# Kernel optimization log

Measured on AMD Instinct MI355X. Metric: run time of the kernel, lower is better.

## Reference

```python
import jax, jax.numpy as jnp
import numpy as np

B, W, L, J, I, O = 512, 1024, 64, 8, 32, 128


def setup_inputs() -> dict:
    key = jax.random.key(0)
    ks = jax.random.split(key, 9)
    wm = jax.random.normal(ks[0], (B, W, L), dtype=jnp.float32)
    constants = jax.random.uniform(ks[1], (J, L), minval=-1.0, maxval=1.0, dtype=jnp.float32)
    gammas = jax.random.uniform(ks[2], (J, L), minval=0.0, maxval=1.0, dtype=jnp.float32)
    body_w = jax.random.normal(ks[3], (J, I, L), dtype=jnp.float32) / np.sqrt(L).astype(np.float32)
    body_b = jax.random.normal(ks[4], (J, I), dtype=jnp.float32) * 0.01
    slot_w = jax.random.normal(ks[5], (J, L * I, L), dtype=jnp.float32) / np.sqrt(L).astype(np.float32)
    slot_b = jax.random.normal(ks[6], (J, L * I), dtype=jnp.float32) * 0.01
    head_w = jax.random.normal(ks[7], (O, I), dtype=jnp.float32) / np.sqrt(I).astype(np.float32)
    head_b = jax.random.normal(ks[8], (O,), dtype=jnp.float32) * 0.01
    return {"working_memory": wm, "constants": constants, "gammas": gammas,
            "body_w": body_w, "body_b": body_b, "slot_w": slot_w, "slot_b": slot_b,
            "head_w": head_w, "head_b": head_b}


def reference(working_memory, constants, gammas, body_w, body_b, slot_w, slot_b, head_w, head_b):
    temperature = 1.0
    g = jnp.clip(gammas, 0.0, 1.0)            # (J,L), torch.clamp equivalent
    w1 = 1.0 - g                               # per-element weight (1-gamma)
    # match_scores[j,b,w] = sum_l w1[j,l] * (c[j,l] - wm[b,w,l])^2, expanded to
    # avoid materializing a (J,B,W,L) intermediate:
    A = jnp.sum(w1 * constants * constants, axis=1)                      # (J,)
    cross = jnp.einsum('jl,bwl->jbw', w1 * constants, working_memory)    # (J,B,W)
    quad = jnp.einsum('jl,bwl->jbw', w1, working_memory * working_memory)
    scores = A[:, None, None] - 2.0 * cross + quad                       # (J,B,W)
    attn = jax.nn.softmax(-scores / temperature, axis=-1)                # (J,B,W)
    best = jnp.einsum('jbw,bwl->jbl', attn, working_memory)              # (J,B,L)
    total_mq = jnp.sum(attn * scores, axis=-1).sum(axis=0)               # (B,)
    # body: per-premise Linear(L->I), scaled by mean clamped gamma
    captured = jnp.einsum('jbl,jil->jbi', best, body_w) + body_b[:, None, :]
    g_avg = g.mean(axis=1)                                               # (J,)
    captured_vars = jnp.einsum('j,jbi->bi', g_avg, captured)             # (B,I)
    # slot selector: per-premise Linear(L -> L*I), softmax over slots,
    # scatter best_props values into slots (the original inner l-loop).
    slot_logits = jnp.einsum('jbl,jkl->jbk', best, slot_w) + slot_b[:, None, :]
    slot_probs = jax.nn.softmax(slot_logits.reshape(J, -1, L, I), axis=-1)
    captured_vars = captured_vars + jnp.einsum('jbli,jbl->bi', slot_probs, best)
    output = captured_vars @ head_w.T + head_b                           # (B,O)
    confidence = jnp.exp(-total_mq)[:, None]                             # (B,1)
    return confidence * output
```

## Files before the change

kernel.cpp:

```cpp
#include <hip/hip_runtime.h>
#include <cstdint>
#include <cstddef>

#define B_ 512
#define W_ 1024
#define L_ 64
#define J_ 8
#define I_ 32
#define O_ 128


__global__ __launch_bounds__(64) void k0_prep(const float* __restrict__ constants,
    const float* __restrict__ gammas, float* __restrict__ wcg,
    float* __restrict__ w1g, float* __restrict__ Ag)
{
  const int l = threadIdx.x;
  #pragma unroll
  for (int j = 0; j < J_; ++j) {
    float g = gammas[j*L_ + l];
    g = fminf(fmaxf(g, 0.f), 1.f);
    float c = constants[j*L_ + l];
    float w1 = 1.f - g;
    w1g[j*L_ + l] = w1;
    wcg[j*L_ + l] = w1 * c;
  }
  if (l < J_) {
    float a = 0.f;
    for (int c = 0; c < L_; ++c) {
      float g = gammas[l*L_ + c];
      g = fminf(fmaxf(g, 0.f), 1.f);
      float cc = constants[l*L_ + c];
      a += (1.f - g) * cc * cc;
    }
    Ag[l] = a;
  }
}

__global__ __launch_bounds__(256, 2) void k12_fused(const float* __restrict__ wm,
    const float* __restrict__ wcg, const float* __restrict__ w1g,
    const float* __restrict__ Ag, float* __restrict__ bpart, float* __restrict__ stats)
{
  __shared__ __align__(16) float xs[128 * 68];
  __shared__ __align__(16) float es[J_ * 128];
  __shared__ float redA[4][4], redB[4][4];
  __shared__ float bcast[J_];

  const int tid = threadIdx.x;
  const int b = blockIdx.x, h = blockIdx.y;
  const int lane = tid & 63, wv = tid >> 6;
  const int w = tid & 127;
  const int jh = tid >> 7;
  const int jbase = __builtin_amdgcn_readfirstlane(jh << 2);
  const int lq = tid & 15, wsl = tid >> 4;

  float accb[J_][4];
  #pragma unroll
  for (int j = 0; j < J_; ++j)
    #pragma unroll
    for (int q = 0; q < 4; ++q) accb[j][q] = 0.f;
  float esum[4], msum[4], m0[4];
  #pragma unroll
  for (int jj = 0; jj < 4; ++jj) { esum[jj] = 0.f; msum[jj] = 0.f; }

  const float* wmb = wm + (size_t)b * (W_*L_) + (size_t)h * (512*L_);

  for (int ch = 0; ch < 4; ++ch) {
    __syncthreads();
    const float4* src = (const float4*)(wmb + ch * (128*L_));
    #pragma unroll
    for (int k = 0; k < 8; ++k) {
      int f = k*256 + tid;
      float4 v = src[f];
      int rw = f >> 4, lw = f & 15;
      *(float4*)&xs[rw*68 + lw*4] = v;
    }
    __syncthreads();

    float a1[4], a2[4];
    #pragma unroll
    for (int jj = 0; jj < 4; ++jj) { a1[jj] = 0.f; a2[jj] = 0.f; }
    #pragma unroll
    for (int c = 0; c < 16; ++c) {
      float4 x = *(const float4*)&xs[w*68 + c*4];
      float4 xq;
      xq.x = x.x*x.x; xq.y = x.y*x.y; xq.z = x.z*x.z; xq.w = x.w*x.w;
      #pragma unroll
      for (int jj = 0; jj < 4; ++jj) {
        float4 wc4 = *(const float4*)(wcg + (jbase+jj)*L_ + c*4);
        float4 w14 = *(const float4*)(w1g + (jbase+jj)*L_ + c*4);
        a1[jj] = fmaf(wc4.x, x.x, a1[jj]);
        a1[jj] = fmaf(wc4.y, x.y, a1[jj]);
        a1[jj] = fmaf(wc4.z, x.z, a1[jj]);
        a1[jj] = fmaf(wc4.w, x.w, a1[jj]);
        a2[jj] = fmaf(w14.x, xq.x, a2[jj]);
        a2[jj] = fmaf(w14.y, xq.y, a2[jj]);
        a2[jj] = fmaf(w14.z, xq.z, a2[jj]);
        a2[jj] = fmaf(w14.w, xq.w, a2[jj]);
      }
    }
    float s[4];
    #pragma unroll
    for (int jj = 0; jj < 4; ++jj)
      s[jj] = Ag[jbase+jj] - 2.f*a1[jj] + a2[jj];

    if (ch == 0) {
      #pragma unroll
      for (int jj = 0; jj < 4; ++jj) {
        float mn = s[jj];
        #pragma unroll
        for (int off = 1; off < 64; off <<= 1)
          mn = fminf(mn, __shfl_xor(mn, off));
        if (lane == 0) redA[wv][jj] = mn;
      }
      __syncthreads();
      if (tid < J_) {
        int jj = tid & 3;
        bcast[tid] = (tid < 4) ? fminf(redA[0][jj], redA[1][jj])
                               : fminf(redA[2][jj], redA[3][jj]);
      }
      __syncthreads();
      #pragma unroll
      for (int jj = 0; jj < 4; ++jj) m0[jj] = bcast[jbase+jj];
    }

    #pragma unroll
    for (int jj = 0; jj < 4; ++jj) {
      float e = __expf(m0[jj] - s[jj]);
      esum[jj] += e;
      msum[jj] = fmaf(e, s[jj], msum[jj]);
      es[(jbase+jj)*128 + w] = e;
    }
    __syncthreads();

    #pragma unroll
    for (int tg = 0; tg < 2; ++tg) {
      float4 x[4];
      #pragma unroll
      for (int t = 0; t < 4; ++t)
        x[t] = *(const float4*)&xs[(wsl*8 + tg*4 + t)*68 + lq*4];
      #pragma unroll
      for (int j = 0; j < J_; ++j) {
        float4 e4 = *(const float4*)&es[j*128 + wsl*8 + tg*4];
        accb[j][0] = fmaf(e4.x, x[0].x, accb[j][0]);
        accb[j][1] = fmaf(e4.x, x[0].y, accb[j][1]);
        accb[j][2] = fmaf(e4.x, x[0].z, accb[j][2]);
        accb[j][3] = fmaf(e4.x, x[0].w, accb[j][3]);
        accb[j][0] = fmaf(e4.y, x[1].x, accb[j][0]);
        accb[j][1] = fmaf(e4.y, x[1].y, accb[j][1]);
        accb[j][2] = fmaf(e4.y, x[1].z, accb[j][2]);
        accb[j][3] = fmaf(e4.y, x[1].w, accb[j][3]);
        accb[j][0] = fmaf(e4.z, x[2].x, accb[j][0]);
        accb[j][1] = fmaf(e4.z, x[2].y, accb[j][1]);
        accb[j][2] = fmaf(e4.z, x[2].z, accb[j][2]);
        accb[j][3] = fmaf(e4.z, x[2].w, accb[j][3]);
        accb[j][0] = fmaf(e4.w, x[3].x, accb[j][0]);
        accb[j][1] = fmaf(e4.w, x[3].y, accb[j][1]);
        accb[j][2] = fmaf(e4.w, x[3].z, accb[j][2]);
        accb[j][3] = fmaf(e4.w, x[3].w, accb[j][3]);
      }
    }
  }

  #pragma unroll
  for (int jj = 0; jj < 4; ++jj) {
    float e = esum[jj], m = msum[jj];
    #pragma unroll
    for (int off = 1; off < 64; off <<= 1) {
      e += __shfl_xor(e, off);
      m += __shfl_xor(m, off);
    }
    if (lane == 0) { redA[wv][jj] = e; redB[wv][jj] = m; }
  }
  __syncthreads();
  if (tid < J_) {
    int jj = tid & 3;
    float E = (tid < 4) ? redA[0][jj] + redA[1][jj] : redA[2][jj] + redA[3][jj];
    float M = (tid < 4) ? redB[0][jj] + redB[1][jj] : redB[2][jj] + redB[3][jj];
    float* st = stats + (((size_t)h*B_ + b)*J_ + tid)*4;
    st[0] = bcast[tid]; st[1] = E; st[2] = M;
  }

  #pragma unroll
  for (int j = 0; j < J_; ++j)
    *(float4*)&xs[((wsl*J_ + j)*16 + lq)*4] = *(float4*)accb[j];
  __syncthreads();
  if (tid < J_*16) {
    int j = tid >> 4, q = tid & 15;
    float4 sum = make_float4(0.f, 0.f, 0.f, 0.f);
    #pragma unroll
    for (int s2 = 0; s2 < 16; ++s2) {
      float4 p = *(const float4*)&xs[((s2*J_ + j)*16 + q)*4];
      sum.x += p.x; sum.y += p.y; sum.z += p.z; sum.w += p.w;
    }
    *(float4*)&bpart[(((size_t)h*J_ + j)*B_ + b)*L_ + q*4] = sum;
  }
}

__global__ __launch_bounds__(128) void k2b_combine(const float* __restrict__ bpart,
    const float* __restrict__ stats, float* __restrict__ best, float* __restrict__ conf)
{
  __shared__ float mred[J_];
  const int b = blockIdx.x, tid = threadIdx.x;
  const int j = tid >> 4, q = tid & 15;
  const float* st0 = stats + ((size_t)b*J_ + j)*4;
  const float* st1 = stats + (((size_t)B_ + b)*J_ + j)*4;
  float m0a = st0[0], E0 = st0[1], M0 = st0[2];
  float m0b = st1[0], E1 = st1[1], M1 = st1[2];
  float M = fminf(m0a, m0b);
  float s0 = __expf(M - m0a), s1 = __expf(M - m0b);
  float E = s0*E0 + s1*E1;
  float inv = 1.f / E;
  float4 p0 = *(const float4*)&bpart[((size_t)j*B_ + b)*L_ + q*4];
  float4 p1 = *(const float4*)&bpart[(((size_t)J_ + j)*B_ + b)*L_ + q*4];
  float4 o;
  o.x = (s0*p0.x + s1*p1.x) * inv;
  o.y = (s0*p0.y + s1*p1.y) * inv;
  o.z = (s0*p0.z + s1*p1.z) * inv;
  o.w = (s0*p0.w + s1*p1.w) * inv;
  *(float4*)&best[((size_t)j*B_ + b)*L_ + q*4] = o;
  if (q == 0) mred[j] = (s0*M0 + s1*M1) * inv;
  __syncthreads();
  if (tid == 0) {
    float mq = 0.f;
    #pragma unroll
    for (int jj = 0; jj < J_; ++jj) mq += mred[jj];
    conf[b] = __expf(-mq);
  }
}

__global__ __launch_bounds__(256) void k3_slot(const float* __restrict__ slot_w,
    const float* __restrict__ slot_b, const float* __restrict__ best,
    float* __restrict__ partial)
{
  const int bx = blockIdx.y;
  const int j = bx >> 3, lg = bx & 7;
  const int bc = blockIdx.x;
  const int tid = threadIdx.x;
  const int wv = tid >> 6, lane = tid & 63;
  const int l2 = lane >> 5, i = lane & 31;
  const int l = lg*8 + wv*2 + l2;
  const int r = l*I_ + i;

  const float* swr = slot_w + ((size_t)j*(L_*I_) + r) * L_;
  float sw[L_];
  #pragma unroll
  for (int c = 0; c < 16; ++c) {
    float4 t = ((const float4*)swr)[c];
    sw[c*4+0] = t.x; sw[c*4+1] = t.y; sw[c*4+2] = t.z; sw[c*4+3] = t.w;
  }
  const float sb = slot_b[j*(L_*I_) + r];
  const float* bestj = best + (size_t)j * B_ * L_;
  float* pout = partial + (size_t)bx * (B_*I_);
  const int lidx = lg*8 + wv*2;

  for (int bi = 0; bi < 32; bi += 4) {
    const int b0 = bc*32 + bi;
    const float* bw[4];
    #pragma unroll
    for (int u = 0; u < 4; ++u) bw[u] = bestj + (size_t)(b0+u) * L_;
    float pa[4], pb[4];
    #pragma unroll
    for (int u = 0; u < 4; ++u) { pa[u] = sb; pb[u] = 0.f; }
    #pragma unroll
    for (int c = 0; c < L_; c += 2) {
      #pragma unroll
      for (int u = 0; u < 4; ++u) {
        pa[u] = fmaf(bw[u][c+0], sw[c+0], pa[u]);
        pb[u] = fmaf(bw[u][c+1], sw[c+1], pb[u]);
      }
    }
    float lgt[4], mx[4], e[4], sm[4];
    #pragma unroll
    for (int u = 0; u < 4; ++u) { lgt[u] = pa[u] + pb[u]; mx[u] = lgt[u]; }
    #pragma unroll
    for (int mask = 16; mask; mask >>= 1)
      #pragma unroll
      for (int u = 0; u < 4; ++u) mx[u] = fmaxf(mx[u], __shfl_xor(mx[u], mask));
    #pragma unroll
    for (int u = 0; u < 4; ++u) { e[u] = __expf(lgt[u] - mx[u]); sm[u] = e[u]; }
    #pragma unroll
    for (int mask = 16; mask; mask >>= 1)
      #pragma unroll
      for (int u = 0; u < 4; ++u) sm[u] += __shfl_xor(sm[u], mask);
    float cv[4];
    #pragma unroll
    for (int u = 0; u < 4; ++u) {
      float bv = l2 ? bw[u][lidx+1] : bw[u][lidx];
      cv[u] = (e[u] / sm[u]) * bv;
    }
    #pragma unroll
    for (int u = 0; u < 4; ++u) cv[u] += __shfl_xor(cv[u], 32);
    if (l2 == 0) {
      #pragma unroll
      for (int u = 0; u < 4; ++u)
        pout[(size_t)(b0+u)*I_ + i] = cv[u];
    }
  }
}

__global__ __launch_bounds__(128) void k4_head(const float* __restrict__ partial,
    const float* __restrict__ best, const float* __restrict__ gammas,
    const float* __restrict__ body_w, const float* __restrict__ body_b,
    const float* __restrict__ head_w, const float* __restrict__ head_b,
    const float* __restrict__ conf, float* __restrict__ out)
{
  __shared__ float gavg[J_];
  __shared__ float cvred[4][I_];
  __shared__ float cvf[I_];
  const int b = blockIdx.x, tid = threadIdx.x;
  const int i = tid & 31, q = tid >> 5;
  if (tid < J_) {
    float gsum = 0.f;
    for (int l = 0; l < L_; ++l) {
      float g = gammas[tid*L_ + l];
      gsum += fminf(fmaxf(g, 0.f), 1.f);
    }
    gavg[tid] = gsum * (1.f / L_);
  }
  __syncthreads();

  float acc = 0.f;
  for (int s = q; s < 64; s += 4)
    acc += partial[((size_t)s*B_ + b)*I_ + i];

  #pragma unroll
  for (int u = 0; u < 2; ++u) {
    const int j = q + u*4;
    const float* bwv  = best + ((size_t)j*B_ + b)*L_;
    const float* wrow = body_w + (size_t)(j*I_ + i)*L_;
    float d0 = body_b[j*I_ + i], d1 = 0.f, d2 = 0.f, d3 = 0.f;
    #pragma unroll
    for (int c = 0; c < L_; c += 4) {
      d0 = fmaf(bwv[c+0], wrow[c+0], d0);
      d1 = fmaf(bwv[c+1], wrow[c+1], d1);
      d2 = fmaf(bwv[c+2], wrow[c+2], d2);
      d3 = fmaf(bwv[c+3], wrow[c+3], d3);
    }
    acc = fmaf(gavg[j], (d0 + d1) + (d2 + d3), acc);
  }
  cvred[q][i] = acc;
  __syncthreads();
  if (tid < I_)
    cvf[i] = cvred[0][i] + cvred[1][i] + cvred[2][i] + cvred[3][i];
  __syncthreads();
  float oacc = head_b[tid];
  #pragma unroll
  for (int i2 = 0; i2 < I_; ++i2) oacc = fmaf(cvf[i2], head_w[tid*I_ + i2], oacc);
  out[(size_t)b*O_ + tid] = conf[b] * oacc;
}

extern "C" void kernel_launch(void* const* d_in, const int* in_sizes, int n_in,
                              void* d_out, int out_size, void* d_ws, size_t ws_size,
                              hipStream_t stream) {
  const float* wm        = (const float*)d_in[0];
  const float* constants = (const float*)d_in[1];
  const float* gammas    = (const float*)d_in[2];
  const float* body_w    = (const float*)d_in[3];
  const float* body_b    = (const float*)d_in[4];
  const float* slot_w    = (const float*)d_in[5];
  const float* slot_b    = (const float*)d_in[6];
  const float* head_w    = (const float*)d_in[7];
  const float* head_b    = (const float*)d_in[8];
  float* out = (float*)d_out;

  float* ws      = (float*)d_ws;
  float* wcg     = ws;
  float* w1g     = wcg + J_*L_;
  float* Ag      = w1g + J_*L_;
  float* best    = Ag + 16;
  float* conf    = best + (size_t)J_*B_*L_;
  float* partial = conf + B_;
  float* bpart   = partial + (size_t)64*B_*I_;
  float* stats   = bpart + (size_t)2*J_*B_*L_;

  hipLaunchKernelGGL(k0_prep, dim3(1), dim3(64), 0, stream,
                     constants, gammas, wcg, w1g, Ag);
  hipLaunchKernelGGL(k12_fused, dim3(B_, 2), dim3(256), 0, stream,
                     wm, wcg, w1g, Ag, bpart, stats);
  hipLaunchKernelGGL(k2b_combine, dim3(B_), dim3(128), 0, stream,
                     bpart, stats, best, conf);
  hipLaunchKernelGGL(k3_slot, dim3(16, 64), dim3(256), 0, stream,
                     slot_w, slot_b, best, partial);
  hipLaunchKernelGGL(k4_head, dim3(B_), dim3(128), 0, stream,
                     partial, best, gammas, body_w, body_b, head_w, head_b, conf, out);
}
```

Measured before the change: 289.1 us.

## Double-buffer wm chunks via async global-to-LDS loads and drop slot softmax max

The fused score/attention kernel now streams working memory in 64-row chunks into a double-buffered, XOR-swizzled shared array using global_load_lds, prefetching the next chunk while the current one is computed. Each wave now owns two premises for its own 64 rows, so the per-chunk min is taken within a wave and the cross-wave min reductions and their extra barriers go away. Separately, the slot softmax skips max subtraction and exponentiates the logits directly, removing a shuffle reduction. That relies on slot logits staying small enough not to overflow. The per-wave minimum differs from the old block minimum, but the combine step rescales by stored minima, so results should stay consistent.

```diff
diff --git a/kernel.cpp b/kernel.cpp
--- a/kernel.cpp
+++ b/kernel.cpp
@@ -9,6 +9,9 @@
 #define I_ 32
 #define O_ 128
 
+
+typedef const __attribute__((address_space(1))) void* gas_ptr;
+typedef __attribute__((address_space(3))) void* las_ptr;
 
 __global__ __launch_bounds__(64) void k0_prep(const float* __restrict__ constants,
     const float* __restrict__ gammas, float* __restrict__ wcg,
@@ -40,156 +43,152 @@
     const float* __restrict__ wcg, const float* __restrict__ w1g,
     const float* __restrict__ Ag, float* __restrict__ bpart, float* __restrict__ stats)
 {
-  __shared__ __align__(16) float xs[128 * 68];
-  __shared__ __align__(16) float es[J_ * 128];
-  __shared__ float redA[4][4], redB[4][4];
-  __shared__ float bcast[J_];
+  __shared__ __align__(16) float xs[2][64 * 64];
+  __shared__ __align__(16) float es[J_ * 64];
 
   const int tid = threadIdx.x;
   const int b = blockIdx.x, h = blockIdx.y;
-  const int lane = tid & 63, wv = tid >> 6;
-  const int w = tid & 127;
-  const int jh = tid >> 7;
-  const int jbase = __builtin_amdgcn_readfirstlane(jh << 2);
+  const int lane = tid & 63;
+  const int wvu = __builtin_amdgcn_readfirstlane(tid >> 6);
+  const int j0  = wvu * 2;
   const int lq = tid & 15, wsl = tid >> 4;
+  const int wm15 = lane & 15;
+  const int rl = lane >> 4, pcg = lane & 15;
+
+  const float* wmb = wm + (size_t)b * (W_*L_) + (size_t)h * (512*L_);
 
   float accb[J_][4];
   #pragma unroll
   for (int j = 0; j < J_; ++j)
     #pragma unroll
     for (int q = 0; q < 4; ++q) accb[j][q] = 0.f;
-  float esum[4], msum[4], m0[4];
-  #pragma unroll
-  for (int jj = 0; jj < 4; ++jj) { esum[jj] = 0.f; msum[jj] = 0.f; }
-
-  const float* wmb = wm + (size_t)b * (W_*L_) + (size_t)h * (512*L_);
-
-  for (int ch = 0; ch < 4; ++ch) {
-    __syncthreads();
-    const float4* src = (const float4*)(wmb + ch * (128*L_));
-    #pragma unroll
-    for (int k = 0; k < 8; ++k) {
-      int f = k*256 + tid;
-      float4 v = src[f];
-      int rw = f >> 4, lw = f & 15;
-      *(float4*)&xs[rw*68 + lw*4] = v;
-    }
-    __syncthreads();
-
-    float a1[4], a2[4];
-    #pragma unroll
-    for (int jj = 0; jj < 4; ++jj) { a1[jj] = 0.f; a2[jj] = 0.f; }
+  float esum[2] = {0.f, 0.f}, msum[2] = {0.f, 0.f}, m0v[2];
+
+  {
+    const float* csrc = wmb;
+    #pragma unroll
+    for (int k = 0; k < 4; ++k) {
+      const int grow = wvu*16 + k*4 + rl;
+      const int lcg  = pcg ^ (k*4 + rl);
+      __builtin_amdgcn_global_load_lds(
+          (gas_ptr)(csrc + grow*64 + lcg*4),
+          (las_ptr)&xs[0][(wvu*16 + k*4)*64], 16, 0, 0);
+    }
+  }
+  __syncthreads();
+
+  for (int ch = 0; ch < 8; ++ch) {
+    const float* xb = &xs[ch & 1][0];
+
+    if (ch < 7) {
+      const float* csrc = wmb + (ch+1) * (64*L_);
+      float* ldst = &xs[(ch+1) & 1][0];
+      #pragma unroll
+      for (int k = 0; k < 4; ++k) {
+        const int grow = wvu*16 + k*4 + rl;
+        const int lcg  = pcg ^ (k*4 + rl);
+        __builtin_amdgcn_global_load_lds(
+            (gas_ptr)(csrc + grow*64 + lcg*4),
+            (las_ptr)(ldst + (wvu*16 + k*4)*64), 16, 0, 0);
+      }
+    }
+
+    float a10 = 0.f, a11 = 0.f, a20 = 0.f, a21 = 0.f;
     #pragma unroll
     for (int c = 0; c < 16; ++c) {
-      float4 x = *(const float4*)&xs[w*68 + c*4];
+      const int col = c ^ wm15;
+      float4 x = *(const float4*)&xb[lane*64 + col*4];
       float4 xq;
       xq.x = x.x*x.x; xq.y = x.y*x.y; xq.z = x.z*x.z; xq.w = x.w*x.w;
-      #pragma unroll
-      for (int jj = 0; jj < 4; ++jj) {
-        float4 wc4 = *(const float4*)(wcg + (jbase+jj)*L_ + c*4);
-        float4 w14 = *(const float4*)(w1g + (jbase+jj)*L_ + c*4);
-        a1[jj] = fmaf(wc4.x, x.x, a1[jj]);
-        a1[jj] = fmaf(wc4.y, x.y, a1[jj]);
-        a1[jj] = fmaf(wc4.z, x.z, a1[jj]);
-        a1[jj] = fmaf(wc4.w, x.w, a1[jj]);
-        a2[jj] = fmaf(w14.x, xq.x, a2[jj]);
-        a2[jj] = fmaf(w14.y, xq.y, a2[jj]);
-        a2[jj] = fmaf(w14.z, xq.z, a2[jj]);
-        a2[jj] = fmaf(w14.w, xq.w, a2[jj]);
+      float4 wc0 = *(const float4*)(wcg + (j0  )*L_ + c*4);
+      float4 wc1 = *(const float4*)(wcg + (j0+1)*L_ + c*4);
+      float4 w10 = *(const float4*)(w1g + (j0  )*L_ + c*4);
+      float4 w11 = *(const float4*)(w1g + (j0+1)*L_ + c*4);
+      a10 = fmaf(wc0.x, x.x, a10); a10 = fmaf(wc0.y, x.y, a10);
+      a10 = fmaf(wc0.z, x.z, a10); a10 = fmaf(wc0.w, x.w, a10);
+      a11 = fmaf(wc1.x, x.x, a11); a11 = fmaf(wc1.y, x.y, a11);
+      a11 = fmaf(wc1.z, x.z, a11); a11 = fmaf(wc1.w, x.w, a11);
+      a20 = fmaf(w10.x, xq.x, a20); a20 = fmaf(w10.y, xq.y, a20);
+      a20 = fmaf(w10.z, xq.z, a20); a20 = fmaf(w10.w, xq.w, a20);
+      a21 = fmaf(w11.x, xq.x, a21); a21 = fmaf(w11.y, xq.y, a21);
+      a21 = fmaf(w11.z, xq.z, a21); a21 = fmaf(w11.w, xq.w, a21);
+    }
+    float s0 = Ag[j0]   - 2.f*a10 + a20;
+    float s1 = Ag[j0+1] - 2.f*a11 + a21;
+
+    if (ch == 0) {
+      float mn0 = s0, mn1 = s1;
+      #pragma unroll
+      for (int off = 1; off < 64; off <<= 1) {
+        mn0 = fminf(mn0, __shfl_xor(mn0, off));
+        mn1 = fminf(mn1, __shfl_xor(mn1, off));
       }
-    }
-    float s[4];
-    #pragma unroll
-    for (int jj = 0; jj < 4; ++jj)
-      s[jj] = Ag[jbase+jj] - 2.f*a1[jj] + a2[jj];
-
-    if (ch == 0) {
-      #pragma unroll
-      for (int jj = 0; jj < 4; ++jj) {
-        float mn = s[jj];
-        #pragma unroll
-        for (int off = 1; off < 64; off <<= 1)
-          mn = fminf(mn, __shfl_xor(mn, off));
-        if (lane == 0) redA[wv][jj] = mn;
-      }
-      __syncthreads();
-      if (tid < J_) {
-        int jj = tid & 3;
-        bcast[tid] = (tid < 4) ? fminf(redA[0][jj], redA[1][jj])
-                               : fminf(redA[2][jj], redA[3][jj]);
-      }
-      __syncthreads();
-      #pragma unroll
-      for (int jj = 0; jj < 4; ++jj) m0[jj] = bcast[jbase+jj];
-    }
-
-    #pragma unroll
-    for (int jj = 0; jj < 4; ++jj) {
-      float e = __expf(m0[jj] - s[jj]);
-      esum[jj] += e;
-      msum[jj] = fmaf(e, s[jj], msum[jj]);
-      es[(jbase+jj)*128 + w] = e;
-    }
+      m0v[0] = mn0; m0v[1] = mn1;
+    }
+
+    float e0 = __expf(m0v[0] - s0);
+    float e1 = __expf(m0v[1] - s1);
+    esum[0] += e0; msum[0] = fmaf(e0, s0, msum[0]);
+    esum[1] += e1; msum[1] = fmaf(e1, s1, msum[1]);
+    es[(j0  )*64 + lane] = e0;
+    es[(j0+1)*64 + lane] = e1;
     __syncthreads();
 
-    #pragma unroll
-    for (int tg = 0; tg < 2; ++tg) {
-      float4 x[4];
-      #pragma unroll
-      for (int t = 0; t < 4; ++t)
-        x[t] = *(const float4*)&xs[(wsl*8 + tg*4 + t)*68 + lq*4];
-      #pragma unroll
-      for (int j = 0; j < J_; ++j) {
-        float4 e4 = *(const float4*)&es[j*128 + wsl*8 + tg*4];
-        accb[j][0] = fmaf(e4.x, x[0].x, accb[j][0]);
-        accb[j][1] = fmaf(e4.x, x[0].y, accb[j][1]);
-        accb[j][2] = fmaf(e4.x, x[0].z, accb[j][2]);
-        accb[j][3] = fmaf(e4.x, x[0].w, accb[j][3]);
-        accb[j][0] = fmaf(e4.y, x[1].x, accb[j][0]);
-        accb[j][1] = fmaf(e4.y, x[1].y, accb[j][1]);
-        accb[j][2] = fmaf(e4.y, x[1].z, accb[j][2]);
-        accb[j][3] = fmaf(e4.y, x[1].w, accb[j][3]);
-        accb[j][0] = fmaf(e4.z, x[2].x, accb[j][0]);
-        accb[j][1] = fmaf(e4.z, x[2].y, accb[j][1]);
-        accb[j][2] = fmaf(e4.z, x[2].z, accb[j][2]);
-        accb[j][3] = fmaf(e4.z, x[2].w, accb[j][3]);
-        accb[j][0] = fmaf(e4.w, x[3].x, accb[j][0]);
-        accb[j][1] = fmaf(e4.w, x[3].y, accb[j][1]);
-        accb[j][2] = fmaf(e4.w, x[3].z, accb[j][2]);
-        accb[j][3] = fmaf(e4.w, x[3].w, accb[j][3]);
-      }
-    }
-  }
-
-  #pragma unroll
-  for (int jj = 0; jj < 4; ++jj) {
-    float e = esum[jj], m = msum[jj];
+    float4 x4[4];
+    #pragma unroll
+    for (int t = 0; t < 4; ++t) {
+      const int w2 = wsl*4 + t;
+      const int col = lq ^ (w2 & 15);
+      x4[t] = *(const float4*)&xb[w2*64 + col*4];
+    }
+    #pragma unroll
+    for (int j = 0; j < J_; ++j) {
+      float4 e4 = *(const float4*)&es[j*64 + wsl*4];
+      accb[j][0] = fmaf(e4.x, x4[0].x, accb[j][0]);
+      accb[j][1] = fmaf(e4.x, x4[0].y, accb[j][1]);
+      accb[j][2] = fmaf(e4.x, x4[0].z, accb[j][2]);
+      accb[j][3] = fmaf(e4.x, x4[0].w, accb[j][3]);
+      accb[j][0] = fmaf(e4.y, x4[1].x, accb[j][0]);
+      accb[j][1] = fmaf(e4.y, x4[1].y, accb[j][1]);
+      accb[j][2] = fmaf(e4.y, x4[1].z, accb[j][2]);
+      accb[j][3] = fmaf(e4.y, x4[1].w, accb[j][3]);
+      accb[j][0] = fmaf(e4.z, x4[2].x, accb[j][0]);
+      accb[j][1] = fmaf(e4.z, x4[2].y, accb[j][1]);
+      accb[j][2] = fmaf(e4.z, x4[2].z, accb[j][2]);
+      accb[j][3] = fmaf(e4.z, x4[2].w, accb[j][3]);
+      accb[j][0] = fmaf(e4.w, x4[3].x, accb[j][0]);
+      accb[j][1] = fmaf(e4.w, x4[3].y, accb[j][1]);
+      accb[j][2] = fmaf(e4.w, x4[3].z, accb[j][2]);
+      accb[j][3] = fmaf(e4.w, x4[3].w, accb[j][3]);
+    }
+    __syncthreads();
+  }
+
+  #pragma unroll
+  for (int u = 0; u < 2; ++u) {
+    float e = esum[u], m = msum[u];
     #pragma unroll
     for (int off = 1; off < 64; off <<= 1) {
       e += __shfl_xor(e, off);
       m += __shfl_xor(m, off);
     }
-    if (lane == 0) { redA[wv][jj] = e; redB[wv][jj] = m; }
-  }
-  __syncthreads();
-  if (tid < J_) {
-    int jj = tid & 3;
-    float E = (tid < 4) ? redA[0][jj] + redA[1][jj] : redA[2][jj] + redA[3][jj];
-    float M = (tid < 4) ? redB[0][jj] + redB[1][jj] : redB[2][jj] + redB[3][jj];
-    float* st = stats + (((size_t)h*B_ + b)*J_ + tid)*4;
-    st[0] = bcast[tid]; st[1] = E; st[2] = M;
-  }
-
+    if (lane == 0) {
+      float* st = stats + (((size_t)h*B_ + b)*J_ + (j0+u))*4;
+      st[0] = m0v[u]; st[1] = e; st[2] = m;
+    }
+  }
+
+  float* xsf = &xs[0][0];
   #pragma unroll
   for (int j = 0; j < J_; ++j)
-    *(float4*)&xs[((wsl*J_ + j)*16 + lq)*4] = *(float4*)accb[j];
+    *(float4*)&xsf[((wsl*J_ + j)*16 + lq)*4] = *(float4*)accb[j];
   __syncthreads();
   if (tid < J_*16) {
     int j = tid >> 4, q = tid & 15;
     float4 sum = make_float4(0.f, 0.f, 0.f, 0.f);
     #pragma unroll
     for (int s2 = 0; s2 < 16; ++s2) {
-      float4 p = *(const float4*)&xs[((s2*J_ + j)*16 + q)*4];
+      float4 p = *(const float4*)&xsf[((s2*J_ + j)*16 + q)*4];
       sum.x += p.x; sum.y += p.y; sum.z += p.z; sum.w += p.w;
     }
     *(float4*)&bpart[(((size_t)h*J_ + j)*B_ + b)*L_ + q*4] = sum;
@@ -269,15 +268,9 @@
         pb[u] = fmaf(bw[u][c+1], sw[c+1], pb[u]);
       }
     }
-    float lgt[4], mx[4], e[4], sm[4];
-    #pragma unroll
-    for (int u = 0; u < 4; ++u) { lgt[u] = pa[u] + pb[u]; mx[u] = lgt[u]; }
-    #pragma unroll
-    for (int mask = 16; mask; mask >>= 1)
-      #pragma unroll
-      for (int u = 0; u < 4; ++u) mx[u] = fmaxf(mx[u], __shfl_xor(mx[u], mask));
-    #pragma unroll
-    for (int u = 0; u < 4; ++u) { e[u] = __expf(lgt[u] - mx[u]); sm[u] = e[u]; }
+    float e[4], sm[4];
+    #pragma unroll
+    for (int u = 0; u < 4; ++u) { e[u] = __expf(pa[u] + pb[u]); sm[u] = e[u]; }
     #pragma unroll
     for (int mask = 16; mask; mask >>= 1)
       #pragma unroll
```

Result: no change. 284.0 us (-1.8%).
